# Kernel tuning notes

Hardware: AMD Instinct MI355X
Metric: run time of the kernel (lower is better)

## Reference

```python
import jax, jax.numpy as jnp
import numpy as np

EPS = 1e-5
H = 128
NA = 300000
NB = 600000
NBRS = 6

def _bn(x, gamma, beta):
    # BatchNorm1d in training mode: batch stats over dim 0, biased variance
    mu = jnp.mean(x, axis=0)
    var = jnp.mean((x - mu) ** 2, axis=0)
    return gamma * (x - mu) * jax.lax.rsqrt(var + EPS) + beta

def _lin(x, w, b):
    return x @ w.T + b

def setup_inputs() -> dict:
    key = jax.random.key(0)
    ks = jax.random.split(key, 20)
    s = 1.0 / np.sqrt(H)
    d = {
        'atom_layer_input': jax.random.normal(ks[0], (NA, H), jnp.float32),
        'bond_layer_input': jax.random.normal(ks[1], (NB, H), jnp.float32),
        'atom_adjacency_graph': jax.random.randint(ks[2], (NA, NBRS), 0, NA, jnp.int32),
        'atom_bond_adjacency_graph': jax.random.randint(ks[3], (NA, NBRS), 0, NB, jnp.int32),
        'bond_atom_adjacency_graph': jax.random.randint(ks[4], (NB, 2), 0, NA, jnp.int32),
    }
    names = ['U', 'V', 'A', 'B', 'C']
    for i, n in enumerate(names):
        d[n + '_w'] = jax.random.uniform(ks[5 + 2 * i], (H, H), jnp.float32, -s, s)
        d[n + '_b'] = jax.random.uniform(ks[6 + 2 * i], (H,), jnp.float32, -s, s)
    d['bn_bond_gamma'] = jnp.ones((H,), jnp.float32)
    d['bn_bond_beta'] = jnp.zeros((H,), jnp.float32)
    d['bn_atom_gamma'] = jnp.ones((H,), jnp.float32)
    d['bn_atom_beta'] = jnp.zeros((H,), jnp.float32)
    return d

def reference(atom_layer_input, bond_layer_input, atom_adjacency_graph,
              atom_bond_adjacency_graph, bond_atom_adjacency_graph,
              U_w, U_b, V_w, V_b, A_w, A_b, B_w, B_b, C_w, C_b,
              bn_bond_gamma, bn_bond_beta, bn_atom_gamma, bn_atom_beta):
    # --- edge (bond) update ---
    ex = atom_layer_input[bond_atom_adjacency_graph[:, 0]]  # [NB, H]
    ey = atom_layer_input[bond_atom_adjacency_graph[:, 1]]  # [NB, H]
    edge_syn = _lin(bond_layer_input, A_w, A_b) + _lin(ex, B_w, B_b) + _lin(ey, C_w, C_b)
    edge_gates = jax.nn.sigmoid(edge_syn)                    # [NB, H]
    edge_syn_bn = _bn(edge_syn, bn_bond_gamma, bn_bond_beta)
    bond_layer_output = jax.nn.relu(edge_syn_bn)             # residual overwritten in source
    # --- node (atom) update ---
    nbr_feats = atom_layer_input[atom_adjacency_graph]       # [NA, 6, H] gather
    nbr_V = jnp.einsum('nkh,oh->nko', nbr_feats, V_w) + V_b  # [NA, 6, H]
    nbr_gates = edge_gates[atom_bond_adjacency_graph]        # [NA, 6, H] gather
    msg = jnp.sum(nbr_gates * nbr_V, axis=1)                 # [NA, H]
    atom_syn = _lin(atom_layer_input, U_w, U_b) + msg
    atom_syn_bn = _bn(atom_syn, bn_atom_gamma, bn_atom_beta)
    atom_layer_output = jax.nn.relu(atom_syn_bn) + atom_layer_input  # residual (atom_feature_dim==0)
    return (atom_layer_output, bond_layer_output)
```

## Files before the change

kernel.cpp:

```cpp
#include <hip/hip_runtime.h>
#include <hip/hip_bf16.h>


#define H   128
#define NA  300000
#define NB  600000
#define EPS 1e-5f

#define NTILE_A (NA / 32)
#define NTILE_B (NB / 32)
#define GRID_A  512
#define GRID_B  1024
#define EGRID   2048
#define LDSW    136

typedef __attribute__((ext_vector_type(4)))  float  f32x4;
typedef __attribute__((ext_vector_type(16))) float  f32x16;
typedef __attribute__((ext_vector_type(8)))  __bf16 bfv8;
typedef __attribute__((ext_vector_type(8)))  unsigned short u16x8;

static __device__ __forceinline__ unsigned short f2bf(float f) {
    unsigned u = __float_as_uint(f);
    u = (u + 0x7fffu + ((u >> 16) & 1u)) >> 16;
    return (unsigned short)u;
}
static __device__ __forceinline__ float bf2f(unsigned short s) {
    return __uint_as_float(((unsigned)s) << 16);
}

static __device__ __forceinline__ bfv8 load_frag(const float* __restrict__ p) {
    f32x4 a = *(const f32x4*)p, b = *(const f32x4*)(p + 4);
    bfv8 f;
#pragma unroll
    for (int i = 0; i < 4; i++) { f[i] = (__bf16)a[i]; f[i + 4] = (__bf16)b[i]; }
    return f;
}

static __device__ __forceinline__ u16x8 pack2(f32x4 a, f32x4 b) {
    u16x8 w;
#pragma unroll
    for (int i = 0; i < 4; i++) { w[i] = f2bf(a[i]); w[i + 4] = f2bf(b[i]); }
    return w;
}

__global__ __launch_bounds__(512, 4) void k_atom_gemm(
    const float* __restrict__ X,
    const float* __restrict__ Uw, const float* __restrict__ Vw,
    const float* __restrict__ Bw, const float* __restrict__ Cw,
    unsigned short* __restrict__ Uxo, unsigned short* __restrict__ Vxo,
    unsigned short* __restrict__ Bxo, unsigned short* __restrict__ Cxo)
{
    __shared__ unsigned short xs[2][32 * LDSW];

    const int tid   = threadIdx.x;
    const int lane  = tid & 63;
    const int w     = tid >> 6;
    const int ng    = w & 3;
    const int pair  = w >> 2;
    const int l31   = lane & 31;
    const int khalf = lane >> 5;

    const int wrow_off = (ng * 32 + l31) * H + khalf * 8;
    const int cperm    = ng * 32 + khalf * 16;

    const float* W0 = pair ? Bw : Uw;
    const float* W1 = pair ? Cw : Vw;
    unsigned short* O0 = pair ? Bxo : Uxo;
    unsigned short* O1 = pair ? Cxo : Vxo;

    bfv8 aw0[8], aw1[8];
#pragma unroll
    for (int k = 0; k < 8; k++) {
        aw0[k] = load_frag(W0 + wrow_off + k * 16);
        aw1[k] = load_frag(W1 + wrow_off + k * 16);
    }

    const int srow = tid >> 4;
    const int sseg = tid & 15;

    const int stride = gridDim.x;
    int t = blockIdx.x;

    f32x4 sl0, sl1;
    {
        const float* sp = X + (size_t)(t * 32 + srow) * H + sseg * 8;
        sl0 = *(const f32x4*)sp; sl1 = *(const f32x4*)(sp + 4);
    }
    *(u16x8*)&xs[0][srow * LDSW + sseg * 8] = pack2(sl0, sl1);
    __syncthreads();

    int p = 0;
#pragma unroll 1
    for (; t < NTILE_A; ) {
        const int tn = t + stride;
        const bool have = tn < NTILE_A;

        if (have) {
            const float* sp = X + (size_t)(tn * 32 + srow) * H + sseg * 8;
            sl0 = *(const f32x4*)sp; sl1 = *(const f32x4*)(sp + 4);
        }

        const unsigned short* xrow = &xs[p][l31 * LDSW + khalf * 8];
        const size_t obase = (size_t)(t * 32 + l31) * H + cperm;

#define DO_WT(AW, OP)                                                          \
        {                                                                      \
            f32x16 acc;                                                        \
            _Pragma("unroll") for (int i = 0; i < 16; i++) acc[i] = 0.0f;      \
            _Pragma("unroll") for (int k = 0; k < 8; k++) {                    \
                bfv8 xf = *(const bfv8*)(xrow + k * 16);                       \
                acc = __builtin_amdgcn_mfma_f32_32x32x16_bf16(AW[k], xf, acc, 0, 0, 0); \
            }                                                                  \
            u16x8 o0, o1;                                                      \
            _Pragma("unroll") for (int v = 0; v < 8; v++) {                    \
                o0[v] = f2bf(acc[v]); o1[v] = f2bf(acc[v + 8]);                \
            }                                                                  \
            *(u16x8*)(OP + obase)     = o0;                                    \
            *(u16x8*)(OP + obase + 8) = o1;                                    \
        }
        DO_WT(aw0, O0)
        DO_WT(aw1, O1)
#undef DO_WT

        if (have)
            *(u16x8*)&xs[p ^ 1][srow * LDSW + sseg * 8] = pack2(sl0, sl1);
        __syncthreads();
        p ^= 1;
        t = tn;
    }
}

__global__ __launch_bounds__(256, 4) void k_bond_gemm(
    const float* __restrict__ Xb,
    const float* __restrict__ Aw, const float* __restrict__ Ab,
    const float* __restrict__ Bb, const float* __restrict__ Cb,
    const int* __restrict__ g2,
    const unsigned short* __restrict__ Bx, const unsigned short* __restrict__ Cx,
    unsigned short* __restrict__ esyn)
{
    __shared__ unsigned short xs[2][32 * LDSW];

    const int tid   = threadIdx.x;
    const int lane  = tid & 63;
    const int ng    = tid >> 6;
    const int l31   = lane & 31;
    const int khalf = lane >> 5;

    const int cperm = ng * 32 + khalf * 16;
    const int cbias = ng * 32 + khalf * 4;

    bfv8 aw[8];
    const float* wr = Aw + (ng * 32 + l31) * H + khalf * 8;
#pragma unroll
    for (int k = 0; k < 8; k++) aw[k] = load_frag(wr + k * 16);

    f32x4 bv[4];
#pragma unroll
    for (int g = 0; g < 4; g++) {
        f32x4 a = *(const f32x4*)(Ab + cbias + g * 8);
        f32x4 b = *(const f32x4*)(Bb + cbias + g * 8);
        f32x4 c = *(const f32x4*)(Cb + cbias + g * 8);
#pragma unroll
        for (int j = 0; j < 4; j++) a[j] += b[j] + c[j];
        bv[g] = a;
    }

    const int srow = tid >> 3;
    const int sseg = tid & 7;

    const int stride = gridDim.x;
    int t = blockIdx.x;

    f32x4 sl[4];
    {
        const float* sp = Xb + (size_t)(t * 32 + srow) * H + sseg * 16;
#pragma unroll
        for (int i = 0; i < 4; i++) sl[i] = *(const f32x4*)(sp + 4 * i);
    }
    {
        unsigned short* d = &xs[0][srow * LDSW + sseg * 16];
        *(u16x8*)d       = pack2(sl[0], sl[1]);
        *(u16x8*)(d + 8) = pack2(sl[2], sl[3]);
    }
    int2 gg = *(const int2*)(g2 + 2 * (size_t)(t * 32 + l31));
    __syncthreads();

    int p = 0;
#pragma unroll 1
    for (; t < NTILE_B; ) {
        const int tn = t + stride;
        const bool have = tn < NTILE_B;

        if (have) {
            const float* sp = Xb + (size_t)(tn * 32 + srow) * H + sseg * 16;
#pragma unroll
            for (int i = 0; i < 4; i++) sl[i] = *(const f32x4*)(sp + 4 * i);
        }

        const unsigned short* bxp = Bx + (size_t)gg.x * H + cperm;
        const unsigned short* cxp = Cx + (size_t)gg.y * H + cperm;
        u16x8 b0 = *(const u16x8*)bxp, b1 = *(const u16x8*)(bxp + 8);
        u16x8 c0 = *(const u16x8*)cxp, c1 = *(const u16x8*)(cxp + 8);
        if (have) gg = *(const int2*)(g2 + 2 * (size_t)(tn * 32 + l31));

        const unsigned short* xrow = &xs[p][l31 * LDSW + khalf * 8];
        f32x16 acc;
#pragma unroll
        for (int i = 0; i < 16; i++) acc[i] = 0.0f;
#pragma unroll
        for (int k = 0; k < 8; k++) {
            bfv8 xf = *(const bfv8*)(xrow + k * 16);
            acc = __builtin_amdgcn_mfma_f32_32x32x16_bf16(aw[k], xf, acc, 0, 0, 0);
        }

        u16x8 o0, o1;
#pragma unroll
        for (int v = 0; v < 8; v++) {
            o0[v] = f2bf(acc[v]     + bv[v >> 2][v & 3]       + bf2f(b0[v]) + bf2f(c0[v]));
            o1[v] = f2bf(acc[v + 8] + bv[2 + (v >> 2)][v & 3] + bf2f(b1[v]) + bf2f(c1[v]));
        }
        unsigned short* op = esyn + (size_t)(t * 32 + l31) * H + cperm;
        *(u16x8*)op       = o0;
        *(u16x8*)(op + 8) = o1;

        if (have) {
            unsigned short* d = &xs[p ^ 1][srow * LDSW + sseg * 16];
            *(u16x8*)d       = pack2(sl[0], sl[1]);
            *(u16x8*)(d + 8) = pack2(sl[2], sl[3]);
        }
        __syncthreads();
        p ^= 1;
        t = tn;
    }
}

__global__ __launch_bounds__(256) void k_col_stats(const unsigned short* __restrict__ buf,
                                                   long nrows,
                                                   float* __restrict__ psum,
                                                   float* __restrict__ psq)
{
    const size_t total  = (size_t)nrows * (H / 8);
    const size_t stride = (size_t)gridDim.x * 256;
    float s[8], q[8];
#pragma unroll
    for (int j = 0; j < 8; j++) { s[j] = 0.f; q[j] = 0.f; }
    for (size_t i = (size_t)blockIdx.x * 256 + threadIdx.x; i < total; i += stride) {
        u16x8 v = ((const u16x8*)buf)[i];
#pragma unroll
        for (int j = 0; j < 8; j++) { float f = bf2f(v[j]); s[j] += f; q[j] += f * f; }
    }
    __shared__ float ls[256][8], lq[256][8];
#pragma unroll
    for (int j = 0; j < 8; j++) { ls[threadIdx.x][j] = s[j]; lq[threadIdx.x][j] = q[j]; }
    __syncthreads();
    if (threadIdx.x < 128) {
        const int c = threadIdx.x, cg = c >> 3, j = c & 7;
        float S = 0.f, Q = 0.f;
        for (int rg = 0; rg < 16; rg++) { S += ls[rg * 16 + cg][j]; Q += lq[rg * 16 + cg][j]; }
        psum[(size_t)blockIdx.x * H + c] = S;
        psq [(size_t)blockIdx.x * H + c] = Q;
    }
}

__global__ void k_bn_stats(const float* __restrict__ psum, const float* __restrict__ psq,
                           int nblk, float invN,
                           const float* __restrict__ gamma, const float* __restrict__ beta,
                           float* __restrict__ scale, float* __restrict__ shift)
{
    __shared__ float ls[256], lq[256];
    const int c = blockIdx.x;
    float s = 0.f, q = 0.f;
    for (int i = threadIdx.x; i < nblk; i += 256) {
        s += psum[(size_t)i * H + c];
        q += psq [(size_t)i * H + c];
    }
    ls[threadIdx.x] = s; lq[threadIdx.x] = q;
    __syncthreads();
    for (int off = 128; off > 0; off >>= 1) {
        if ((int)threadIdx.x < off) {
            ls[threadIdx.x] += ls[threadIdx.x + off];
            lq[threadIdx.x] += lq[threadIdx.x + off];
        }
        __syncthreads();
    }
    if (threadIdx.x == 0) {
        const int r = c & 31, kh = r >> 4, wi = r & 15;
        const int ct = (c & ~31) + (wi >> 2) * 8 + kh * 4 + (wi & 3);
        float mean = ls[0] * invN;
        float var  = lq[0] * invN - mean * mean;
        float sc   = gamma[ct] * rsqrtf(var + EPS);
        scale[c] = sc;
        shift[c] = beta[ct] - mean * sc;
    }
}

__global__ __launch_bounds__(256) void k_bond_out(const unsigned short* __restrict__ esyn,
                                                  float* __restrict__ y,
                                                  const float* __restrict__ scale,
                                                  const float* __restrict__ shift)
{
    const size_t total  = (size_t)NB * (H / 8);
    const size_t stride = (size_t)gridDim.x * 256;
    const int c0 = (threadIdx.x & 15) * 8;
    const f32x4 sc0 = *(const f32x4*)(scale + c0), sc1 = *(const f32x4*)(scale + c0 + 4);
    const f32x4 sh0 = *(const f32x4*)(shift + c0), sh1 = *(const f32x4*)(shift + c0 + 4);
    const int tc0 = (c0 & ~31) + (((c0 >> 2) & 3) * 8) + ((c0 >> 4) & 1) * 4;
    const int tc1 = tc0 + 8;
    for (size_t i = (size_t)blockIdx.x * 256 + threadIdx.x; i < total; i += stride) {
        u16x8 v = ((const u16x8*)esyn)[i];
        const size_t row = i >> 4;
        f32x4 o0, o1;
#pragma unroll
        for (int j = 0; j < 4; j++) {
            o0[j] = fmaxf(bf2f(v[j])     * sc0[j] + sh0[j], 0.0f);
            o1[j] = fmaxf(bf2f(v[j + 4]) * sc1[j] + sh1[j], 0.0f);
        }
        float* yp = y + row * H;
        *(f32x4*)(yp + tc0) = o0;
        *(f32x4*)(yp + tc1) = o1;
    }
}

__global__ __launch_bounds__(256) void k_atom_msg(
    const unsigned short* __restrict__ Ux,
    const unsigned short* __restrict__ Vx,
    const unsigned short* __restrict__ esyn,
    const int* __restrict__ adj,
    const int* __restrict__ abadj,
    const float* __restrict__ Ub, const float* __restrict__ Vb,
    unsigned short* __restrict__ syn_a,
    float* __restrict__ psum, float* __restrict__ psq)
{
    const int cg = threadIdx.x & 15;
    const int rh = threadIdx.x >> 4;
    const int c0 = cg * 8;
    const int tc0 = (c0 & ~31) + (((c0 >> 2) & 3) * 8) + ((c0 >> 4) & 1) * 4;
    const f32x4 ub0 = *(const f32x4*)(Ub + tc0), ub1 = *(const f32x4*)(Ub + tc0 + 8);
    const f32x4 vb0 = *(const f32x4*)(Vb + tc0), vb1 = *(const f32x4*)(Vb + tc0 + 8);

    float s[8], q[8];
#pragma unroll
    for (int j = 0; j < 8; j++) { s[j] = 0.f; q[j] = 0.f; }

    const int rstride = gridDim.x * 16;
    int r = blockIdx.x * 16 + rh;

    int2 A[3], Bv[3];
    if (r < NA) {
#pragma unroll
        for (int p = 0; p < 3; p++) {
            A[p]  = *(const int2*)(adj   + (size_t)r * 6 + 2 * p);
            Bv[p] = *(const int2*)(abadj + (size_t)r * 6 + 2 * p);
        }
    }

#pragma unroll 1
    for (; r < NA; ) {
        const int rn = r + rstride;

        const int ai[6] = {A[0].x, A[0].y, A[1].x, A[1].y, A[2].x, A[2].y};
        const int bi[6] = {Bv[0].x, Bv[0].y, Bv[1].x, Bv[1].y, Bv[2].x, Bv[2].y};

        u16x8 uv = *(const u16x8*)(Ux + (size_t)r * H + c0);

        if (rn < NA) {
#pragma unroll
            for (int p = 0; p < 3; p++) {
                A[p]  = *(const int2*)(adj   + (size_t)rn * 6 + 2 * p);
                Bv[p] = *(const int2*)(abadj + (size_t)rn * 6 + 2 * p);
            }
        }

        float v[8];
#pragma unroll
        for (int j = 0; j < 4; j++) {
            v[j]     = bf2f(uv[j])     + ub0[j];
            v[j + 4] = bf2f(uv[j + 4]) + ub1[j];
        }
#pragma unroll
        for (int k = 0; k < 6; k++) {
            u16x8 vx = *(const u16x8*)(Vx   + (size_t)ai[k] * H + c0);
            u16x8 es = *(const u16x8*)(esyn + (size_t)bi[k] * H + c0);
#pragma unroll
            for (int j = 0; j < 4; j++) {
                float g0 = 1.0f / (1.0f + __expf(-bf2f(es[j])));
                float g1 = 1.0f / (1.0f + __expf(-bf2f(es[j + 4])));
                v[j]     += g0 * (bf2f(vx[j])     + vb0[j]);
                v[j + 4] += g1 * (bf2f(vx[j + 4]) + vb1[j]);
            }
        }
        u16x8 ov;
#pragma unroll
        for (int j = 0; j < 8; j++) ov[j] = f2bf(v[j]);
        *(u16x8*)(syn_a + (size_t)r * H + c0) = ov;
#pragma unroll
        for (int j = 0; j < 8; j++) { s[j] += v[j]; q[j] += v[j] * v[j]; }

        r = rn;
    }

    __shared__ float ls[256][8], lq[256][8];
#pragma unroll
    for (int j = 0; j < 8; j++) { ls[threadIdx.x][j] = s[j]; lq[threadIdx.x][j] = q[j]; }
    __syncthreads();
    if (threadIdx.x < 128) {
        const int c = threadIdx.x, g = c >> 3, j = c & 7;
        float S = 0.f, Q = 0.f;
        for (int rg = 0; rg < 16; rg++) { S += ls[rg * 16 + g][j]; Q += lq[rg * 16 + g][j]; }
        psum[(size_t)blockIdx.x * H + c] = S;
        psq [(size_t)blockIdx.x * H + c] = Q;
    }
}

__global__ __launch_bounds__(256) void k_atom_out(const unsigned short* __restrict__ syn,
                                                  const float* __restrict__ xin,
                                                  float* __restrict__ y,
                                                  const float* __restrict__ scale,
                                                  const float* __restrict__ shift)
{
    const size_t total  = (size_t)NA * (H / 8);
    const size_t stride = (size_t)gridDim.x * 256;
    const int c0 = (threadIdx.x & 15) * 8;
    const f32x4 sc0 = *(const f32x4*)(scale + c0), sc1 = *(const f32x4*)(scale + c0 + 4);
    const f32x4 sh0 = *(const f32x4*)(shift + c0), sh1 = *(const f32x4*)(shift + c0 + 4);
    const int tc0 = (c0 & ~31) + (((c0 >> 2) & 3) * 8) + ((c0 >> 4) & 1) * 4;
    const int tc1 = tc0 + 8;
    for (size_t i = (size_t)blockIdx.x * 256 + threadIdx.x; i < total; i += stride) {
        u16x8 v = ((const u16x8*)syn)[i];
        const size_t row = i >> 4;
        const float* xp = xin + row * H;
        f32x4 x0 = *(const f32x4*)(xp + tc0), x1 = *(const f32x4*)(xp + tc1);
        f32x4 o0, o1;
#pragma unroll
        for (int j = 0; j < 4; j++) {
            o0[j] = fmaxf(bf2f(v[j])     * sc0[j] + sh0[j], 0.0f) + x0[j];
            o1[j] = fmaxf(bf2f(v[j + 4]) * sc1[j] + sh1[j], 0.0f) + x1[j];
        }
        float* yp = y + row * H;
        *(f32x4*)(yp + tc0) = o0;
        *(f32x4*)(yp + tc1) = o1;
    }
}

extern "C" void kernel_launch(void* const* d_in, const int* in_sizes, int n_in,
                              void* d_out, int out_size, void* d_ws, size_t ws_size,
                              hipStream_t stream)
{
    const float* X     = (const float*)d_in[0];
    const float* Xb    = (const float*)d_in[1];
    const int*   adj   = (const int*)d_in[2];
    const int*   abadj = (const int*)d_in[3];
    const int*   g2    = (const int*)d_in[4];
    const float* Uw = (const float*)d_in[5],  *Ub = (const float*)d_in[6];
    const float* Vw = (const float*)d_in[7],  *Vb = (const float*)d_in[8];
    const float* Aw = (const float*)d_in[9],  *Ab = (const float*)d_in[10];
    const float* Bw = (const float*)d_in[11], *Bb = (const float*)d_in[12];
    const float* Cw = (const float*)d_in[13], *Cb = (const float*)d_in[14];
    const float* gb = (const float*)d_in[15], *bb = (const float*)d_in[16];
    const float* ga = (const float*)d_in[17], *ba = (const float*)d_in[18];

    float* out_atom = (float*)d_out;
    float* out_bond = out_atom + (size_t)NA * H;

    char* ws = (char*)d_ws;
    size_t o = 0;
    unsigned short* Ux    = (unsigned short*)(ws + o); o += (size_t)NA * H * 2;
    unsigned short* Vx    = (unsigned short*)(ws + o); o += (size_t)NA * H * 2;
    unsigned short* Bx    = (unsigned short*)(ws + o); o += (size_t)NA * H * 2;
    unsigned short* Cx    = (unsigned short*)(ws + o); o += (size_t)NA * H * 2;
    unsigned short* esyn  = (unsigned short*)(ws + o); o += (size_t)NB * H * 2;
    unsigned short* syn_a = (unsigned short*)(ws + o); o += (size_t)NA * H * 2;
    float* psum_b = (float*)(ws + o);  o += (size_t)EGRID * H * 4;
    float* psq_b  = (float*)(ws + o);  o += (size_t)EGRID * H * 4;
    float* psum_a = (float*)(ws + o);  o += (size_t)EGRID * H * 4;
    float* psq_a  = (float*)(ws + o);  o += (size_t)EGRID * H * 4;
    float* scale_b = (float*)(ws + o); o += 512;
    float* shift_b = (float*)(ws + o); o += 512;
    float* scale_a = (float*)(ws + o); o += 512;
    float* shift_a = (float*)(ws + o); o += 512;
    (void)o; (void)ws_size; (void)in_sizes; (void)n_in; (void)out_size;

    k_atom_gemm<<<GRID_A, 512, 0, stream>>>(X, Uw, Vw, Bw, Cw, Ux, Vx, Bx, Cx);
    k_bond_gemm<<<GRID_B, 256, 0, stream>>>(Xb, Aw, Ab, Bb, Cb, g2, Bx, Cx, esyn);
    k_col_stats<<<EGRID, 256, 0, stream>>>(esyn, NB, psum_b, psq_b);
    k_bn_stats<<<H, 256, 0, stream>>>(psum_b, psq_b, EGRID, 1.0f / NB, gb, bb, scale_b, shift_b);
    k_bond_out<<<EGRID, 256, 0, stream>>>(esyn, out_bond, scale_b, shift_b);
    k_atom_msg<<<EGRID, 256, 0, stream>>>(Ux, Vx, esyn, adj, abadj, Ub, Vb, syn_a, psum_a, psq_a);
    k_bn_stats<<<H, 256, 0, stream>>>(psum_a, psq_a, EGRID, 1.0f / NA, ga, ba, scale_a, shift_a);
    k_atom_out<<<EGRID, 256, 0, stream>>>(syn_a, X, out_atom, scale_a, shift_a);
}
```

Before: 649.8 us.

## Fuse bond BN column stats into bond GEMM and stage GEMM outputs through LDS

```diff
diff --git a/kernel.cpp b/kernel.cpp
--- a/kernel.cpp
+++ b/kernel.cpp
@@ -28,19 +28,19 @@
     return __uint_as_float(((unsigned)s) << 16);
 }
 
+static __device__ __forceinline__ u16x8 pack2(f32x4 a, f32x4 b) {
+    u16x8 w;
+#pragma unroll
+    for (int i = 0; i < 4; i++) { w[i] = f2bf(a[i]); w[i + 4] = f2bf(b[i]); }
+    return w;
+}
+
 static __device__ __forceinline__ bfv8 load_frag(const float* __restrict__ p) {
     f32x4 a = *(const f32x4*)p, b = *(const f32x4*)(p + 4);
     bfv8 f;
 #pragma unroll
     for (int i = 0; i < 4; i++) { f[i] = (__bf16)a[i]; f[i + 4] = (__bf16)b[i]; }
     return f;
-}
-
-static __device__ __forceinline__ u16x8 pack2(f32x4 a, f32x4 b) {
-    u16x8 w;
-#pragma unroll
-    for (int i = 0; i < 4; i++) { w[i] = f2bf(a[i]); w[i + 4] = f2bf(b[i]); }
-    return w;
 }
 
 __global__ __launch_bounds__(512, 4) void k_atom_gemm(
@@ -51,6 +51,7 @@
     unsigned short* __restrict__ Bxo, unsigned short* __restrict__ Cxo)
 {
     __shared__ unsigned short xs[2][32 * LDSW];
+    __shared__ unsigned short es[2][32 * LDSW];
 
     const int tid   = threadIdx.x;
     const int lane  = tid & 63;
@@ -65,8 +66,6 @@
 
     const float* W0 = pair ? Bw : Uw;
     const float* W1 = pair ? Cw : Vw;
-    unsigned short* O0 = pair ? Bxo : Uxo;
-    unsigned short* O1 = pair ? Cxo : Vxo;
 
     bfv8 aw0[8], aw1[8];
 #pragma unroll
@@ -75,8 +74,11 @@
         aw1[k] = load_frag(W1 + wrow_off + k * 16);
     }
 
-    const int srow = tid >> 4;
-    const int sseg = tid & 15;
+    const int srow = tid >> 4, sseg = tid & 15;
+    const int g = tid >> 8, ft = tid & 255;
+    const int frow = ft >> 3, fseg = ft & 7;
+    unsigned short* O0 = g ? Bxo : Uxo;
+    unsigned short* O1 = g ? Cxo : Vxo;
 
     const int stride = gridDim.x;
     int t = blockIdx.x;
@@ -94,34 +96,62 @@
     for (; t < NTILE_A; ) {
         const int tn = t + stride;
         const bool have = tn < NTILE_A;
-
         if (have) {
             const float* sp = X + (size_t)(tn * 32 + srow) * H + sseg * 8;
             sl0 = *(const f32x4*)sp; sl1 = *(const f32x4*)(sp + 4);
         }
 
         const unsigned short* xrow = &xs[p][l31 * LDSW + khalf * 8];
-        const size_t obase = (size_t)(t * 32 + l31) * H + cperm;
-
-#define DO_WT(AW, OP)                                                          \
-        {                                                                      \
-            f32x16 acc;                                                        \
-            _Pragma("unroll") for (int i = 0; i < 16; i++) acc[i] = 0.0f;      \
-            _Pragma("unroll") for (int k = 0; k < 8; k++) {                    \
-                bfv8 xf = *(const bfv8*)(xrow + k * 16);                       \
-                acc = __builtin_amdgcn_mfma_f32_32x32x16_bf16(AW[k], xf, acc, 0, 0, 0); \
-            }                                                                  \
-            u16x8 o0, o1;                                                      \
-            _Pragma("unroll") for (int v = 0; v < 8; v++) {                    \
-                o0[v] = f2bf(acc[v]); o1[v] = f2bf(acc[v + 8]);                \
-            }                                                                  \
-            *(u16x8*)(OP + obase)     = o0;                                    \
-            *(u16x8*)(OP + obase + 8) = o1;                                    \
-        }
-        DO_WT(aw0, O0)
-        DO_WT(aw1, O1)
-#undef DO_WT
-
+        unsigned short*       esw  = &es[pair][l31 * LDSW + cperm];
+        const unsigned short* esr  = &es[g][frow * LDSW + fseg * 16];
+        const size_t fbase = (size_t)(t * 32 + frow) * H + fseg * 16;
+
+        {
+            f32x16 acc;
+#pragma unroll
+            for (int i = 0; i < 16; i++) acc[i] = 0.0f;
+#pragma unroll
+            for (int k = 0; k < 8; k++) {
+                bfv8 xf = *(const bfv8*)(xrow + k * 16);
+                acc = __builtin_amdgcn_mfma_f32_32x32x16_bf16(aw0[k], xf, acc, 0, 0, 0);
+            }
+            u16x8 o0, o1;
+#pragma unroll
+            for (int v = 0; v < 8; v++) { o0[v] = f2bf(acc[v]); o1[v] = f2bf(acc[v + 8]); }
+            *(u16x8*)esw       = o0;
+            *(u16x8*)(esw + 8) = o1;
+        }
+        __syncthreads();
+
+        f32x16 acc1;
+#pragma unroll
+        for (int i = 0; i < 16; i++) acc1[i] = 0.0f;
+#pragma unroll
+        for (int k = 0; k < 8; k++) {
+            bfv8 xf = *(const bfv8*)(xrow + k * 16);
+            acc1 = __builtin_amdgcn_mfma_f32_32x32x16_bf16(aw1[k], xf, acc1, 0, 0, 0);
+        }
+        {
+            u16x8 e0 = *(const u16x8*)esr, e1 = *(const u16x8*)(esr + 8);
+            *(u16x8*)(O0 + fbase)     = e0;
+            *(u16x8*)(O0 + fbase + 8) = e1;
+        }
+        __syncthreads();
+
+        {
+            u16x8 o0, o1;
+#pragma unroll
+            for (int v = 0; v < 8; v++) { o0[v] = f2bf(acc1[v]); o1[v] = f2bf(acc1[v + 8]); }
+            *(u16x8*)esw       = o0;
+            *(u16x8*)(esw + 8) = o1;
+        }
+        __syncthreads();
+
+        {
+            u16x8 e0 = *(const u16x8*)esr, e1 = *(const u16x8*)(esr + 8);
+            *(u16x8*)(O1 + fbase)     = e0;
+            *(u16x8*)(O1 + fbase + 8) = e1;
+        }
         if (have)
             *(u16x8*)&xs[p ^ 1][srow * LDSW + sseg * 8] = pack2(sl0, sl1);
         __syncthreads();
@@ -136,37 +166,37 @@
     const float* __restrict__ Bb, const float* __restrict__ Cb,
     const int* __restrict__ g2,
     const unsigned short* __restrict__ Bx, const unsigned short* __restrict__ Cx,
-    unsigned short* __restrict__ esyn)
+    unsigned short* __restrict__ esyn,
+    float* __restrict__ psum, float* __restrict__ psq)
 {
     __shared__ unsigned short xs[2][32 * LDSW];
+    __shared__ unsigned short es[32 * LDSW];
+    __shared__ float bias_s[128];
 
     const int tid   = threadIdx.x;
     const int lane  = tid & 63;
     const int ng    = tid >> 6;
     const int l31   = lane & 31;
     const int khalf = lane >> 5;
-
     const int cperm = ng * 32 + khalf * 16;
-    const int cbias = ng * 32 + khalf * 4;
 
     bfv8 aw[8];
     const float* wr = Aw + (ng * 32 + l31) * H + khalf * 8;
 #pragma unroll
     for (int k = 0; k < 8; k++) aw[k] = load_frag(wr + k * 16);
 
-    f32x4 bv[4];
-#pragma unroll
-    for (int g = 0; g < 4; g++) {
-        f32x4 a = *(const f32x4*)(Ab + cbias + g * 8);
-        f32x4 b = *(const f32x4*)(Bb + cbias + g * 8);
-        f32x4 c = *(const f32x4*)(Cb + cbias + g * 8);
-#pragma unroll
-        for (int j = 0; j < 4; j++) a[j] += b[j] + c[j];
-        bv[g] = a;
-    }
-
-    const int srow = tid >> 3;
-    const int sseg = tid & 7;
+    if (tid < 128) {
+        const int pcol = tid;
+        const int grp = pcol >> 5, r = pcol & 31, kh = r >> 4, wi = r & 15;
+        const int ct = grp * 32 + (wi >> 2) * 8 + kh * 4 + (wi & 3);
+        bias_s[pcol] = Ab[ct] + Bb[ct] + Cb[ct];
+    }
+
+    const int srow = tid >> 3, sseg = tid & 7;
+
+    float fs[16], fq[16];
+#pragma unroll
+    for (int i = 0; i < 16; i++) { fs[i] = 0.f; fq[i] = 0.f; }
 
     const int stride = gridDim.x;
     int t = blockIdx.x;
@@ -182,7 +212,7 @@
         *(u16x8*)d       = pack2(sl[0], sl[1]);
         *(u16x8*)(d + 8) = pack2(sl[2], sl[3]);
     }
-    int2 gg = *(const int2*)(g2 + 2 * (size_t)(t * 32 + l31));
+    int2 ggf = *(const int2*)(g2 + 2 * (size_t)(t * 32 + srow));
     __syncthreads();
 
     int p = 0;
@@ -197,31 +227,50 @@
             for (int i = 0; i < 4; i++) sl[i] = *(const f32x4*)(sp + 4 * i);
         }
 
-        const unsigned short* bxp = Bx + (size_t)gg.x * H + cperm;
-        const unsigned short* cxp = Cx + (size_t)gg.y * H + cperm;
+        {
+            const unsigned short* xrow = &xs[p][l31 * LDSW + khalf * 8];
+            f32x16 acc;
+#pragma unroll
+            for (int i = 0; i < 16; i++) acc[i] = 0.0f;
+#pragma unroll
+            for (int k = 0; k < 8; k++) {
+                bfv8 xf = *(const bfv8*)(xrow + k * 16);
+                acc = __builtin_amdgcn_mfma_f32_32x32x16_bf16(aw[k], xf, acc, 0, 0, 0);
+            }
+            u16x8 o0, o1;
+#pragma unroll
+            for (int v = 0; v < 8; v++) { o0[v] = f2bf(acc[v]); o1[v] = f2bf(acc[v + 8]); }
+            unsigned short* esw = &es[l31 * LDSW + cperm];
+            *(u16x8*)esw       = o0;
+            *(u16x8*)(esw + 8) = o1;
+        }
+
+        const unsigned short* bxp = Bx + (size_t)ggf.x * H + sseg * 16;
+        const unsigned short* cxp = Cx + (size_t)ggf.y * H + sseg * 16;
         u16x8 b0 = *(const u16x8*)bxp, b1 = *(const u16x8*)(bxp + 8);
         u16x8 c0 = *(const u16x8*)cxp, c1 = *(const u16x8*)(cxp + 8);
-        if (have) gg = *(const int2*)(g2 + 2 * (size_t)(tn * 32 + l31));
-
-        const unsigned short* xrow = &xs[p][l31 * LDSW + khalf * 8];
-        f32x16 acc;
-#pragma unroll
-        for (int i = 0; i < 16; i++) acc[i] = 0.0f;
-#pragma unroll
-        for (int k = 0; k < 8; k++) {
-            bfv8 xf = *(const bfv8*)(xrow + k * 16);
-            acc = __builtin_amdgcn_mfma_f32_32x32x16_bf16(aw[k], xf, acc, 0, 0, 0);
-        }
-
-        u16x8 o0, o1;
-#pragma unroll
-        for (int v = 0; v < 8; v++) {
-            o0[v] = f2bf(acc[v]     + bv[v >> 2][v & 3]       + bf2f(b0[v]) + bf2f(c0[v]));
-            o1[v] = f2bf(acc[v + 8] + bv[2 + (v >> 2)][v & 3] + bf2f(b1[v]) + bf2f(c1[v]));
-        }
-        unsigned short* op = esyn + (size_t)(t * 32 + l31) * H + cperm;
-        *(u16x8*)op       = o0;
-        *(u16x8*)(op + 8) = o1;
+        if (have) ggf = *(const int2*)(g2 + 2 * (size_t)(tn * 32 + srow));
+        __syncthreads();
+
+        {
+            const unsigned short* esr = &es[srow * LDSW + sseg * 16];
+            u16x8 e0 = *(const u16x8*)esr, e1 = *(const u16x8*)(esr + 8);
+            const float* bp = bias_s + sseg * 16;
+            u16x8 w0, w1;
+#pragma unroll
+            for (int i = 0; i < 8; i++) {
+                float v = bf2f(e0[i]) + bp[i] + bf2f(b0[i]) + bf2f(c0[i]);
+                w0[i] = f2bf(v); fs[i] += v; fq[i] += v * v;
+            }
+#pragma unroll
+            for (int i = 0; i < 8; i++) {
+                float v = bf2f(e1[i]) + bp[8 + i] + bf2f(b1[i]) + bf2f(c1[i]);
+                w1[i] = f2bf(v); fs[8 + i] += v; fq[8 + i] += v * v;
+            }
+            unsigned short* op = esyn + (size_t)(t * 32 + srow) * H + sseg * 16;
+            *(u16x8*)op       = w0;
+            *(u16x8*)(op + 8) = w1;
+        }
 
         if (have) {
             unsigned short* d = &xs[p ^ 1][srow * LDSW + sseg * 16];
@@ -232,33 +281,18 @@
         p ^= 1;
         t = tn;
     }
-}
-
-__global__ __launch_bounds__(256) void k_col_stats(const unsigned short* __restrict__ buf,
-                                                   long nrows,
-                                                   float* __restrict__ psum,
-                                                   float* __restrict__ psq)
-{
-    const size_t total  = (size_t)nrows * (H / 8);
-    const size_t stride = (size_t)gridDim.x * 256;
-    float s[8], q[8];
-#pragma unroll
-    for (int j = 0; j < 8; j++) { s[j] = 0.f; q[j] = 0.f; }
-    for (size_t i = (size_t)blockIdx.x * 256 + threadIdx.x; i < total; i += stride) {
-        u16x8 v = ((const u16x8*)buf)[i];
-#pragma unroll
-        for (int j = 0; j < 8; j++) { float f = bf2f(v[j]); s[j] += f; q[j] += f * f; }
-    }
-    __shared__ float ls[256][8], lq[256][8];
-#pragma unroll
-    for (int j = 0; j < 8; j++) { ls[threadIdx.x][j] = s[j]; lq[threadIdx.x][j] = q[j]; }
-    __syncthreads();
-    if (threadIdx.x < 128) {
-        const int c = threadIdx.x, cg = c >> 3, j = c & 7;
-        float S = 0.f, Q = 0.f;
-        for (int rg = 0; rg < 16; rg++) { S += ls[rg * 16 + cg][j]; Q += lq[rg * 16 + cg][j]; }
-        psum[(size_t)blockIdx.x * H + c] = S;
-        psq [(size_t)blockIdx.x * H + c] = Q;
+
+    float* red = (float*)es;
+    for (int i = 0; i < 16; i++) {
+        __syncthreads();
+        red[tid] = fs[i]; red[256 + tid] = fq[i];
+        __syncthreads();
+        if (tid < 8) {
+            float S = 0.f, Q = 0.f;
+            for (int r = 0; r < 32; r++) { S += red[r * 8 + tid]; Q += red[256 + r * 8 + tid]; }
+            psum[(size_t)blockIdx.x * H + tid * 16 + i] = S;
+            psq [(size_t)blockIdx.x * H + tid * 16 + i] = Q;
+        }
     }
 }
 
@@ -481,9 +515,9 @@
     (void)o; (void)ws_size; (void)in_sizes; (void)n_in; (void)out_size;
 
     k_atom_gemm<<<GRID_A, 512, 0, stream>>>(X, Uw, Vw, Bw, Cw, Ux, Vx, Bx, Cx);
-    k_bond_gemm<<<GRID_B, 256, 0, stream>>>(Xb, Aw, Ab, Bb, Cb, g2, Bx, Cx, esyn);
-    k_col_stats<<<EGRID, 256, 0, stream>>>(esyn, NB, psum_b, psq_b);
-    k_bn_stats<<<H, 256, 0, stream>>>(psum_b, psq_b, EGRID, 1.0f / NB, gb, bb, scale_b, shift_b);
+    k_bond_gemm<<<GRID_B, 256, 0, stream>>>(Xb, Aw, Ab, Bb, Cb, g2, Bx, Cx, esyn,
+                                            psum_b, psq_b);
+    k_bn_stats<<<H, 256, 0, stream>>>(psum_b, psq_b, GRID_B, 1.0f / NB, gb, bb, scale_b, shift_b);
     k_bond_out<<<EGRID, 256, 0, stream>>>(esyn, out_bond, scale_b, shift_b);
     k_atom_msg<<<EGRID, 256, 0, stream>>>(Ux, Vx, esyn, adj, abadj, Ub, Vb, syn_a, psum_a, psq_a);
     k_bn_stats<<<H, 256, 0, stream>>>(psum_a, psq_a, EGRID, 1.0f / NA, ga, ba, scale_a, shift_a);
```

Result: faster. 604.3 us (-7.0%).
